# Kernel optimization log

Measured on AMD Instinct MI355X. Metric: run time of the kernel, lower is better.

Reference implementation:

```python
import jax, jax.numpy as jnp
import numpy as np
import math

N_HEADS = 16


def setup_inputs() -> dict:
    key = jax.random.key(0)
    ks = jax.random.split(key, 6)
    B, S, D = 2, 2048, 2048
    hd = D // N_HEADS  # 128
    scale = 0.02
    x = jax.random.normal(ks[0], (B, S, D), dtype=jnp.float32)
    wq = jax.random.normal(ks[1], (D, D), dtype=jnp.float32) * scale
    wk = jax.random.normal(ks[2], (D, D), dtype=jnp.float32) * scale
    wv = jax.random.normal(ks[3], (D, D), dtype=jnp.float32) * scale
    wo = jax.random.normal(ks[4], (D, D), dtype=jnp.float32) * scale
    # Rotary frequencies: theta = 10000^(-2i/hd), angle[t, i] = t * theta_i
    inv_freq = 1.0 / (10000.0 ** (jnp.arange(0, hd, 2, dtype=jnp.float32) / hd))  # [hd//2]
    angles = jnp.arange(S, dtype=jnp.float32)[:, None] * inv_freq[None, :]  # [S, hd//2]
    freqs_cos = jnp.cos(angles)
    freqs_sin = jnp.sin(angles)
    # Causal additive mask [1,1,S,S]
    causal = jnp.tril(jnp.ones((S, S), dtype=bool))
    mask = jnp.where(causal, 0.0, -1e9).astype(jnp.float32)[None, None]
    return {"x": x, "wq": wq, "wk": wk, "wv": wv, "wo": wo,
            "freqs_cos": freqs_cos, "freqs_sin": freqs_sin, "mask": mask}


def _apply_rope(t, cos, sin):
    # t: [B,S,H,hd]; cos/sin: [S, hd//2]. Complex mult on (even, odd) pairs.
    B, S, H, hd = t.shape
    tr = t.reshape(B, S, H, hd // 2, 2)
    t0, t1 = tr[..., 0], tr[..., 1]
    c = cos[None, :, None, :]
    s = sin[None, :, None, :]
    o0 = t0 * c - t1 * s
    o1 = t0 * s + t1 * c
    return jnp.stack([o0, o1], axis=-1).reshape(B, S, H, hd)


def reference(x, wq, wk, wv, wo, freqs_cos, freqs_sin, mask):
    B, S, D = x.shape
    H = N_HEADS
    hd = D // H
    # Projections (torch Linear: y = x @ W^T)
    q = jnp.einsum('bsd,ed->bse', x, wq).reshape(B, S, H, hd)
    k = jnp.einsum('bsd,ed->bse', x, wk).reshape(B, S, H, hd)
    v = jnp.einsum('bsd,ed->bse', x, wv).reshape(B, S, H, hd)
    q = _apply_rope(q, freqs_cos, freqs_sin)
    k = _apply_rope(k, freqs_cos, freqs_sin)
    # Attention: scores [B,H,S,S]
    scores = jnp.einsum('bshd,bthd->bhst', q, k) / math.sqrt(hd)
    scores = scores + mask[:, :, :S, :S]
    attn = jax.nn.softmax(scores.astype(jnp.float32), axis=-1).astype(q.dtype)
    out = jnp.einsum('bhst,bthd->bshd', attn, v).reshape(B, S, D)
    return jnp.einsum('bsd,ed->bse', out, wo)
```

## Files before the change

kernel.cpp:

```cpp
#include <hip/hip_runtime.h>

typedef unsigned short u16;
typedef __attribute__((ext_vector_type(8))) short short8;
typedef __attribute__((ext_vector_type(4))) short short4s;
typedef __attribute__((ext_vector_type(4))) float f32x4;

__device__ __forceinline__ u16 f2b(float f) {
  union { float f; unsigned u; } c; c.f = f;
  unsigned u = c.u;
  unsigned r = (u + 0x7FFFu + ((u >> 16) & 1u)) >> 16;
  return (u16)r;
}
__device__ __forceinline__ float b2f(u16 h) {
  union { unsigned u; float f; } c; c.u = ((unsigned)h) << 16;
  return c.f;
}

__device__ __forceinline__ void gload16(const u16* g, u16* l) {
  __builtin_amdgcn_global_load_lds((const __attribute__((address_space(1))) void*)g,
                                   (__attribute__((address_space(3))) void*)l, 16, 0, 0);
}

__device__ __forceinline__ short4s tr16(const u16* p) {
  short4s d;
  asm volatile("ds_read_b64_tr_b16 %0, %1"
               : "=v"(d)
               : "v"((const __attribute__((address_space(3))) u16*)p));
  return d;
}

#define MFMA(a, b, c) __builtin_amdgcn_mfma_f32_16x16x32_bf16(a, b, c, 0, 0, 0)

__global__ __launch_bounds__(256) void cast_all(const float* __restrict__ x,
                                                const float* __restrict__ wq,
                                                const float* __restrict__ wk,
                                                const float* __restrict__ wv,
                                                const float* __restrict__ wo,
                                                u16* __restrict__ xb,
                                                u16* __restrict__ wqkv,
                                                u16* __restrict__ wob) {
  int i = blockIdx.x * 256 + threadIdx.x;
  const float4* s; u16* d; int off;
  if (i < 2097152)      { s = (const float4*)x;  d = xb;            off = i; }
  else if (i < 3145728) { s = (const float4*)wq; d = wqkv;          off = i - 2097152; }
  else if (i < 4194304) { s = (const float4*)wk; d = wqkv + 4194304; off = i - 3145728; }
  else if (i < 5242880) { s = (const float4*)wv; d = wqkv + 8388608; off = i - 4194304; }
  else                  { s = (const float4*)wo; d = wob;           off = i - 5242880; }
  float4 v = s[off];
  ushort4 r;
  r.x = f2b(v.x); r.y = f2b(v.y); r.z = f2b(v.z); r.w = f2b(v.w);
  *(ushort4*)(d + (size_t)off * 4) = r;
}

__global__ __launch_bounds__(256) void rope_k(u16* __restrict__ qkv,
                                              const float* __restrict__ fc,
                                              const float* __restrict__ fs) {
  int idx = blockIdx.x * 256 + threadIdx.x;
  int m = idx >> 8;
  int c = idx & 255;
  int s = m & 2047;
  int i0 = (c * 4) & 63;
  u16* p = qkv + (size_t)m * 6144 + 2048 + c * 8;
  short8 v = *(short8*)p;
  float4 cs = *(const float4*)(fc + (size_t)s * 64 + i0);
  float4 sn = *(const float4*)(fs + (size_t)s * 64 + i0);
  float cc[4] = {cs.x, cs.y, cs.z, cs.w};
  float ss[4] = {sn.x, sn.y, sn.z, sn.w};
#pragma unroll
  for (int t = 0; t < 4; ++t) {
    float x0 = b2f((u16)v[2 * t]);
    float x1 = b2f((u16)v[2 * t + 1]);
    float o0 = x0 * cc[t] - x1 * ss[t];
    float o1 = x0 * ss[t] + x1 * cc[t];
    v[2 * t]     = (short)f2b(o0);
    v[2 * t + 1] = (short)f2b(o1);
  }
  *(short8*)p = v;
}

template <int F32OUT>
__global__ __launch_bounds__(512, 2) void gemm_wide(const u16* __restrict__ Ag,
                                                    const u16* __restrict__ Bg,
                                                    void* __restrict__ Cp,
                                                    int M, int N, int K) {
  __shared__ __align__(16) u16 lds[40960];
  const int tid = threadIdx.x;
  const int l = tid & 63, w = tid >> 6;
  const int wm = w >> 2, wn = w & 3;
  const int ln = l & 15, lk = l >> 4;
  const int nbn = N / 384;
  const int nwg = (M >> 8) * nbn;
  const int wg = ((blockIdx.x & 7) * (nwg >> 3)) + (blockIdx.x >> 3);
  const int row0 = (wg / nbn) << 8;
  const int col0 = (wg % nbn) * 384;
  const int T = K >> 5;

#define STAGE_A(t)                                                                     \
  {                                                                                    \
    _Pragma("unroll")                                                                  \
    for (int u = 0; u < 2; ++u) {                                                      \
      int e = u * 512 + tid;                                                           \
      int rr = e >> 2;                                                                 \
      gload16(Ag + (size_t)(row0 + rr) * K + (t) * 32 +                                \
                  (((e & 3) ^ ((rr >> 1) & 3)) << 3),                                  \
              lds + ((t) & 1) * 8192 + e * 8);                                         \
    }                                                                                  \
  }
#define STAGE_B(t)                                                                     \
  {                                                                                    \
    _Pragma("unroll")                                                                  \
    for (int u = 0; u < 3; ++u) {                                                      \
      int e = u * 512 + tid;                                                           \
      int rr = e >> 2;                                                                 \
      gload16(Bg + (size_t)(col0 + rr) * K + (t) * 32 +                                \
                  (((e & 3) ^ ((rr >> 1) & 3)) << 3),                                  \
              lds + 16384 + ((t) & 1) * 12288 + e * 8);                                \
    }                                                                                  \
  }

  f32x4 acc[8][6];
#pragma unroll
  for (int m = 0; m < 8; ++m)
#pragma unroll
    for (int n = 0; n < 6; ++n) acc[m][n] = (f32x4){0.f, 0.f, 0.f, 0.f};

  const int cx = (lk ^ ((ln >> 1) & 3)) << 3;

  STAGE_B(0); STAGE_A(0); STAGE_B(1);
  asm volatile("s_waitcnt vmcnt(3)" ::: "memory");
  __builtin_amdgcn_s_barrier();

  for (int t = 0; t < T; ++t) {
    const u16* aB = lds + (t & 1) * 8192;
    const u16* bB = lds + 16384 + (t & 1) * 12288;
    short8 bf[6];
    short8 af[4];

#pragma unroll
    for (int n = 0; n < 6; ++n)
      bf[n] = *(const short8*)&bB[(wn * 96 + n * 16 + ln) * 32 + cx];
#pragma unroll
    for (int mf = 0; mf < 4; ++mf)
      af[mf] = *(const short8*)&aB[(wm * 128 + mf * 16 + ln) * 32 + cx];
    if (t + 1 < T) STAGE_A(t + 1);
    __builtin_amdgcn_s_setprio(1);
#pragma unroll
    for (int mf = 0; mf < 4; ++mf)
#pragma unroll
      for (int n = 0; n < 6; ++n)
        acc[mf][n] = MFMA(af[mf], bf[n], acc[mf][n]);
    __builtin_amdgcn_s_setprio(0);
    __builtin_amdgcn_s_barrier();

#pragma unroll
    for (int mf = 0; mf < 4; ++mf)
      af[mf] = *(const short8*)&aB[(wm * 128 + (4 + mf) * 16 + ln) * 32 + cx];
    if (t + 2 < T) STAGE_B(t + 2);
    __builtin_amdgcn_s_setprio(1);
#pragma unroll
    for (int mf = 0; mf < 4; ++mf)
#pragma unroll
      for (int n = 0; n < 6; ++n)
        acc[4 + mf][n] = MFMA(af[mf], bf[n], acc[4 + mf][n]);
    __builtin_amdgcn_s_setprio(0);
    if (t + 2 < T) { asm volatile("s_waitcnt vmcnt(3)" ::: "memory"); }
    else           { asm volatile("s_waitcnt vmcnt(0)" ::: "memory"); }
    __builtin_amdgcn_s_barrier();
  }

#pragma unroll
  for (int m = 0; m < 8; ++m) {
    int r0 = row0 + wm * 128 + m * 16 + lk * 4;
#pragma unroll
    for (int n = 0; n < 6; ++n) {
      int cc = col0 + wn * 96 + n * 16 + ln;
#pragma unroll
      for (int j = 0; j < 4; ++j) {
        float v = acc[m][n][j];
        if (F32OUT) ((float*)Cp)[(size_t)(r0 + j) * N + cc] = v;
        else        ((u16*)Cp)[(size_t)(r0 + j) * N + cc]   = f2b(v);
      }
    }
  }
#undef STAGE_A
#undef STAGE_B
}

template <int NREP, int F32OUT>
__global__ __launch_bounds__(512, 2) void gemm_big(const u16* __restrict__ Ag,
                                                   const u16* __restrict__ Bg,
                                                   void* __restrict__ Cp,
                                                   int M, int N, int K) {
  __shared__ __align__(16) u16 lds[32768 + NREP * 8192];
  const int tid = threadIdx.x;
  const int l = tid & 63, w = tid >> 6;
  const int wm = w >> 2, wn = w & 3;
  const int ln = l & 15, lk = l >> 4;
  const int BN = NREP * 64;
  const int nbn = N / BN;
  const int nwg = (M >> 8) * nbn;
  const int wg = ((blockIdx.x & 7) * (nwg >> 3)) + (blockIdx.x >> 3);
  const int row0 = (wg / nbn) << 8;
  const int col0 = (wg % nbn) * BN;
  const int T = K >> 6;

#define STAGE_A(t, h)                                                                  \
  {                                                                                    \
    _Pragma("unroll")                                                                  \
    for (int u = 0; u < 2; ++u) {                                                      \
      int e = u * 512 + tid;                                                           \
      int rr = (h) * 128 + (e >> 3);                                                   \
      gload16(Ag + (size_t)(row0 + rr) * K + (t) * 64 + (((e & 7) ^ (rr & 7)) << 3),   \
              lds + ((t) & 1) * 16384 + (h) * 8192 + e * 8);                           \
    }                                                                                  \
  }
#define STAGE_B(t, pb)                                                                 \
  {                                                                                    \
    int rr = (pb) * 64 + (tid >> 3);                                                   \
    gload16(Bg + (size_t)(col0 + rr) * K + (t) * 64 + (((tid & 7) ^ (rr & 7)) << 3),   \
            lds + 32768 + ((t) & 1) * NREP * 4096 + (pb) * 4096 + tid * 8);            \
  }

  f32x4 acc[8][NREP];
#pragma unroll
  for (int m = 0; m < 8; ++m)
#pragma unroll
    for (int n = 0; n < NREP; ++n) acc[m][n] = (f32x4){0.f, 0.f, 0.f, 0.f};

  const int x = ln & 7;
  const int c0 = (lk ^ x) << 3;
  const int c1 = ((4 + lk) ^ x) << 3;

#pragma unroll
  for (int pb = 0; pb < NREP; ++pb) STAGE_B(0, pb);
  STAGE_A(0, 0); STAGE_A(0, 1);
#pragma unroll
  for (int pb = 0; pb < NREP; ++pb) STAGE_B(1, pb);
  asm volatile("s_waitcnt vmcnt(2)" ::: "memory");
  __builtin_amdgcn_s_barrier();

  for (int t = 0; t < T; ++t) {
    const u16* aB = lds + (t & 1) * 16384 + wm * 8192;
    const u16* bB = lds + 32768 + (t & 1) * NREP * 4096;
    short8 bf[NREP][2];
#pragma unroll
    for (int p = 0; p < 4; ++p) {
      if (p == 0) {
#pragma unroll
        for (int n = 0; n < NREP; ++n) {
          int rb = (wn * NREP * 16 + n * 16 + ln) * 64;
          bf[n][0] = *(const short8*)&bB[rb + c0];
          bf[n][1] = *(const short8*)&bB[rb + c1];
        }
      }
      short8 af[2][2];
#pragma unroll
      for (int m2 = 0; m2 < 2; ++m2) {
        int ra = ((p * 2 + m2) * 16 + ln) * 64;
        af[m2][0] = *(const short8*)&aB[ra + c0];
        af[m2][1] = *(const short8*)&aB[ra + c1];
      }
      if (p == 0)      { if (t + 1 < T) STAGE_A(t + 1, 0); }
      else if (p == 1) { if (t + 1 < T) STAGE_A(t + 1, 1);
                         if (t + 2 < T) STAGE_B(t + 2, 0); }
      else if (p == 2) { if (t + 2 < T) STAGE_B(t + 2, 1); }

      __builtin_amdgcn_s_setprio(1);
#pragma unroll
      for (int m2 = 0; m2 < 2; ++m2)
#pragma unroll
        for (int n = 0; n < NREP; ++n)
#pragma unroll
          for (int kk = 0; kk < 2; ++kk)
            acc[p * 2 + m2][n] = MFMA(af[m2][kk], bf[n][kk], acc[p * 2 + m2][n]);
      __builtin_amdgcn_s_setprio(0);

      if (p == 3) {
        if (t + 2 < T)      { asm volatile("s_waitcnt vmcnt(2)" ::: "memory"); }
        else if (t + 1 < T) { asm volatile("s_waitcnt vmcnt(0)" ::: "memory"); }
      }
      __builtin_amdgcn_s_barrier();
    }
  }

#pragma unroll
  for (int m = 0; m < 8; ++m) {
    int r0 = row0 + wm * 128 + m * 16 + lk * 4;
#pragma unroll
    for (int n = 0; n < NREP; ++n) {
      int cc = col0 + wn * NREP * 16 + n * 16 + ln;
#pragma unroll
      for (int j = 0; j < 4; ++j) {
        float v = acc[m][n][j];
        if (F32OUT) ((float*)Cp)[(size_t)(r0 + j) * N + cc] = v;
        else        ((u16*)Cp)[(size_t)(r0 + j) * N + cc]   = f2b(v);
      }
    }
  }
#undef STAGE_A
#undef STAGE_B
}

__global__ __launch_bounds__(512) void attn_fwd(const u16* __restrict__ qkv,
                                                const float* __restrict__ fc,
                                                const float* __restrict__ fs,
                                                u16* __restrict__ out) {
  __shared__ __align__(16) u16 sK[2][64 * 128];
  __shared__ __align__(16) u16 sV[2][64 * 128];
  __shared__ __align__(16) u16 sP[8][16 * 72];
  const int tid = threadIdx.x, l = tid & 63, w = tid >> 6;
  const int ln = l & 15, lk = l >> 4;

  const int bid = blockIdx.x;
  const int l0 = ((bid & 7) << 5) | (bid >> 3);
  const int bh = l0 >> 3, pr = l0 & 7;
  const int b = bh >> 4, h = bh & 15;

  const u16* Kp = qkv + (size_t)b * 2048 * 6144 + 2048 + h * 128;
  const u16* Vp = Kp + 2048;
  const float scale = 0.08838834764831845f;

  for (int pass = 0; pass < 2; ++pass) {
    const int qt = pass ? (15 - pr) : pr;
    const int m0 = b * 2048 + qt * 128;
    const u16* Qp = qkv + (size_t)m0 * 6144 + h * 128;
    const int srow = qt * 128 + w * 16 + ln;

    short8 qf[4];
#pragma unroll
    for (int kc = 0; kc < 4; ++kc) {
      short8 raw = *(const short8*)(Qp + (size_t)(w * 16 + ln) * 6144 + kc * 32 + lk * 8);
      float4 c4 = *(const float4*)(fc + (size_t)srow * 64 + kc * 16 + lk * 4);
      float4 s4 = *(const float4*)(fs + (size_t)srow * 64 + kc * 16 + lk * 4);
      float cc[4] = {c4.x * scale, c4.y * scale, c4.z * scale, c4.w * scale};
      float ss[4] = {s4.x * scale, s4.y * scale, s4.z * scale, s4.w * scale};
#pragma unroll
      for (int t = 0; t < 4; ++t) {
        float x0 = b2f((u16)raw[2 * t]);
        float x1 = b2f((u16)raw[2 * t + 1]);
        qf[kc][2 * t]     = (short)f2b(x0 * cc[t] - x1 * ss[t]);
        qf[kc][2 * t + 1] = (short)f2b(x0 * ss[t] + x1 * cc[t]);
      }
    }

    f32x4 o[8];
#pragma unroll
    for (int d = 0; d < 8; ++d) o[d] = (f32x4){0.f, 0.f, 0.f, 0.f};
    float mrow[4] = {-1e9f, -1e9f, -1e9f, -1e9f};
    float lsum[4] = {0.f, 0.f, 0.f, 0.f};

    const int ntl = 2 * qt + 2;

    {
#pragma unroll
      for (int q = 0; q < 2; ++q) {
        int e = q * 512 + tid;
        int r = e >> 4, p = e & 15;
        gload16(Kp + (size_t)r * 6144 + ((p ^ (r & 7)) << 3), &sK[0][e * 8]);
        int j = ((e >> 6) << 2) + ((e & 7) >> 1);
        int d = (((e >> 3) & 7) << 4) + ((e & 1) << 3);
        gload16(Vp + (size_t)j * 6144 + d, &sV[0][e * 8]);
      }
    }
    __syncthreads();

    int cur = 0;
    for (int jt = 0; jt < ntl; ++jt) {
      if (jt + 1 < ntl) {
        const u16* Kt = Kp + (size_t)(jt + 1) * 64 * 6144;
        const u16* Vt = Vp + (size_t)(jt + 1) * 64 * 6144;
        int nb = cur ^ 1;
#pragma unroll
        for (int q = 0; q < 2; ++q) {
          int e = q * 512 + tid;
          int r = e >> 4, p = e & 15;
          gload16(Kt + (size_t)r * 6144 + ((p ^ (r & 7)) << 3), &sK[nb][e * 8]);
          int j = ((e >> 6) << 2) + ((e & 7) >> 1);
          int d = (((e >> 3) & 7) << 4) + ((e & 1) << 3);
          gload16(Vt + (size_t)j * 6144 + d, &sV[nb][e * 8]);
        }
      }

      f32x4 sf[4];
      __builtin_amdgcn_s_setprio(1);
#pragma unroll
      for (int nc = 0; nc < 4; ++nc) {
        f32x4 s = (f32x4){0.f, 0.f, 0.f, 0.f};
#pragma unroll
        for (int kc = 0; kc < 4; ++kc) {
          int r = nc * 16 + ln;
          short8 kb = *(const short8*)&sK[cur][r * 128 + (((kc << 2) + lk) ^ (r & 7)) * 8];
          s = MFMA(qf[kc], kb, s);
        }
        sf[nc] = s;
      }
      __builtin_amdgcn_s_setprio(0);

      if (jt >= 2 * qt) {
        int ig = qt * 128 + w * 16 + lk * 4;
#pragma unroll
        for (int nc = 0; nc < 4; ++nc) {
          int jg = jt * 64 + nc * 16 + ln;
#pragma unroll
          for (int j = 0; j < 4; ++j)
            sf[nc][j] = (jg > ig + j) ? -1e9f : sf[nc][j];
        }
      }

      float tm[4];
#pragma unroll
      for (int j = 0; j < 4; ++j)
        tm[j] = fmaxf(fmaxf(sf[0][j], sf[1][j]), fmaxf(sf[2][j], sf[3][j]));
      int ok = (tm[0] <= mrow[0] + 8.f) & (tm[1] <= mrow[1] + 8.f) &
               (tm[2] <= mrow[2] + 8.f) & (tm[3] <= mrow[3] + 8.f);
      if (!__all(ok)) {
#pragma unroll
        for (int off = 1; off < 16; off <<= 1)
#pragma unroll
          for (int j = 0; j < 4; ++j) tm[j] = fmaxf(tm[j], __shfl_xor(tm[j], off, 16));
        float al[4];
#pragma unroll
        for (int j = 0; j < 4; ++j) {
          float nm = fmaxf(mrow[j], tm[j]);
          al[j] = __expf(mrow[j] - nm);
          mrow[j] = nm;
        }
#pragma unroll
        for (int d = 0; d < 8; ++d)
#pragma unroll
          for (int j = 0; j < 4; ++j) o[d][j] *= al[j];
#pragma unroll
        for (int j = 0; j < 4; ++j) lsum[j] *= al[j];
      }

#pragma unroll
      for (int nc = 0; nc < 4; ++nc)
#pragma unroll
        for (int j = 0; j < 4; ++j) {
          float p = __expf(sf[nc][j] - mrow[j]);
          u16 pb = f2b(p);
          sP[w][(lk * 4 + j) * 72 + nc * 16 + ln] = pb;
          lsum[j] += b2f(pb);
        }

      short8 pa0 = *(const short8*)&sP[w][ln * 72 + lk * 8];
      short8 pa1 = *(const short8*)&sP[w][ln * 72 + 32 + lk * 8];
      asm volatile("s_waitcnt lgkmcnt(0)" ::: "memory");
      __builtin_amdgcn_sched_barrier(0);

      short4s tb[4][4];
#define TRISSUE(dblk, slot)                                                  \
      {                                                                      \
        const u16* vb = &sV[cur][(lk * 2) * 512 + (dblk) * 64 + ln * 4];     \
        tb[slot][0] = tr16(vb);                                              \
        tb[slot][1] = tr16(vb + 512);                                        \
        tb[slot][2] = tr16(vb + 4096);                                       \
        tb[slot][3] = tr16(vb + 4096 + 512);                                 \
      }
      TRISSUE(0, 0);
      TRISSUE(1, 1);
      __builtin_amdgcn_s_setprio(1);
#pragma unroll
      for (int d = 0; d < 8; ++d) {
        if (d < 6) TRISSUE(d + 2, (d + 2) & 3);
        if (d < 6)       asm volatile("s_waitcnt lgkmcnt(8)" ::: "memory");
        else if (d == 6) asm volatile("s_waitcnt lgkmcnt(4)" ::: "memory");
        else             asm volatile("s_waitcnt lgkmcnt(0)" ::: "memory");
        __builtin_amdgcn_sched_barrier(0);
        short8 vb0 = {tb[d & 3][0][0], tb[d & 3][0][1], tb[d & 3][0][2], tb[d & 3][0][3],
                      tb[d & 3][1][0], tb[d & 3][1][1], tb[d & 3][1][2], tb[d & 3][1][3]};
        short8 vb1 = {tb[d & 3][2][0], tb[d & 3][2][1], tb[d & 3][2][2], tb[d & 3][2][3],
                      tb[d & 3][3][0], tb[d & 3][3][1], tb[d & 3][3][2], tb[d & 3][3][3]};
        o[d] = MFMA(pa0, vb0, o[d]);
        o[d] = MFMA(pa1, vb1, o[d]);
      }
      __builtin_amdgcn_s_setprio(0);
#undef TRISSUE

      __syncthreads();
      cur ^= 1;
    }

#pragma unroll
    for (int off = 1; off < 16; off <<= 1)
#pragma unroll
      for (int j = 0; j < 4; ++j) lsum[j] += __shfl_xor(lsum[j], off, 16);
    float inv[4];
#pragma unroll
    for (int j = 0; j < 4; ++j) inv[j] = 1.f / lsum[j];
#pragma unroll
    for (int d = 0; d < 8; ++d)
#pragma unroll
      for (int j = 0; j < 4; ++j)
        out[(size_t)(m0 + w * 16 + lk * 4 + j) * 2048 + h * 128 + d * 16 + ln] =
            f2b(o[d][j] * inv[j]);
  }
}

extern "C" void kernel_launch(void* const* d_in, const int* in_sizes, int n_in,
                              void* d_out, int out_size, void* d_ws, size_t ws_size,
                              hipStream_t stream) {
  const float* x  = (const float*)d_in[0];
  const float* wq = (const float*)d_in[1];
  const float* wk = (const float*)d_in[2];
  const float* wv = (const float*)d_in[3];
  const float* wo = (const float*)d_in[4];
  const float* fc = (const float*)d_in[5];
  const float* fs = (const float*)d_in[6];

  char* ws = (char*)d_ws;
  u16* xb   = (u16*)(ws);
  u16* wqkv = (u16*)(ws + 16777216);
  u16* wob  = (u16*)(ws + 41943040);
  u16* qkv  = (u16*)(ws + 50331648);
  u16* aout = (u16*)(ws + 100663296);

  cast_all<<<24576, 256, 0, stream>>>(x, wq, wk, wv, wo, xb, wqkv, wob);
  gemm_wide<0><<<256, 512, 0, stream>>>(xb, wqkv, qkv, 4096, 6144, 2048);
  rope_k<<<4096, 256, 0, stream>>>(qkv, fc, fs);
  attn_fwd<<<256, 512, 0, stream>>>(qkv, fc, fs, aout);
  gemm_big<2, 1><<<256, 512, 0, stream>>>(aout, wob, d_out, 4096, 2048, 2048);
}
```

Baseline: 239.8 us.

## Split attention into one block per query tile with single-buffered K

The attention kernel now launches one block per (batch, head, query tile) instead of pairing two tiles per block, ordering heavy tiles first. K is single-buffered with a mid-loop barrier before its next-tile prefetch, which cuts LDS use so more blocks fit per CU (launch_bounds min-blocks hint of 4). The P tile is written with the library bf16 conversion and lsum accumulates unrounded p. This trades more blocks and an extra barrier per iteration for higher occupancy and better load balance, and normalisation differs slightly from the rounded P used in the MFMA.

```diff
diff --git a/kernel.cpp b/kernel.cpp
--- a/kernel.cpp
+++ b/kernel.cpp
@@ -1,4 +1,5 @@
 #include <hip/hip_runtime.h>
+#include <hip/hip_bf16.h>
 
 typedef unsigned short u16;
 typedef __attribute__((ext_vector_type(8))) short short8;
@@ -301,200 +302,209 @@
 #undef STAGE_B
 }
 
-__global__ __launch_bounds__(512) void attn_fwd(const u16* __restrict__ qkv,
-                                                const float* __restrict__ fc,
-                                                const float* __restrict__ fs,
-                                                u16* __restrict__ out) {
-  __shared__ __align__(16) u16 sK[2][64 * 128];
+__global__ __launch_bounds__(512, 4) void attn_fwd(const u16* __restrict__ qkv,
+                                                   const float* __restrict__ fc,
+                                                   const float* __restrict__ fs,
+                                                   u16* __restrict__ out) {
+  __shared__ __align__(16) u16 sK[64 * 128];
   __shared__ __align__(16) u16 sV[2][64 * 128];
   __shared__ __align__(16) u16 sP[8][16 * 72];
   const int tid = threadIdx.x, l = tid & 63, w = tid >> 6;
   const int ln = l & 15, lk = l >> 4;
 
   const int bid = blockIdx.x;
-  const int l0 = ((bid & 7) << 5) | (bid >> 3);
-  const int bh = l0 >> 3, pr = l0 & 7;
+  const int l0 = ((bid & 7) << 6) | (bid >> 3);
+  const int bh = l0 >> 4;
+  const int qt = 15 - (l0 & 15);
   const int b = bh >> 4, h = bh & 15;
 
   const u16* Kp = qkv + (size_t)b * 2048 * 6144 + 2048 + h * 128;
   const u16* Vp = Kp + 2048;
   const float scale = 0.08838834764831845f;
 
-  for (int pass = 0; pass < 2; ++pass) {
-    const int qt = pass ? (15 - pr) : pr;
-    const int m0 = b * 2048 + qt * 128;
-    const u16* Qp = qkv + (size_t)m0 * 6144 + h * 128;
-    const int srow = qt * 128 + w * 16 + ln;
-
-    short8 qf[4];
-#pragma unroll
-    for (int kc = 0; kc < 4; ++kc) {
-      short8 raw = *(const short8*)(Qp + (size_t)(w * 16 + ln) * 6144 + kc * 32 + lk * 8);
-      float4 c4 = *(const float4*)(fc + (size_t)srow * 64 + kc * 16 + lk * 4);
-      float4 s4 = *(const float4*)(fs + (size_t)srow * 64 + kc * 16 + lk * 4);
-      float cc[4] = {c4.x * scale, c4.y * scale, c4.z * scale, c4.w * scale};
-      float ss[4] = {s4.x * scale, s4.y * scale, s4.z * scale, s4.w * scale};
-#pragma unroll
-      for (int t = 0; t < 4; ++t) {
-        float x0 = b2f((u16)raw[2 * t]);
-        float x1 = b2f((u16)raw[2 * t + 1]);
-        qf[kc][2 * t]     = (short)f2b(x0 * cc[t] - x1 * ss[t]);
-        qf[kc][2 * t + 1] = (short)f2b(x0 * ss[t] + x1 * cc[t]);
-      }
-    }
-
-    f32x4 o[8];
-#pragma unroll
-    for (int d = 0; d < 8; ++d) o[d] = (f32x4){0.f, 0.f, 0.f, 0.f};
-    float mrow[4] = {-1e9f, -1e9f, -1e9f, -1e9f};
-    float lsum[4] = {0.f, 0.f, 0.f, 0.f};
-
-    const int ntl = 2 * qt + 2;
-
-    {
+  const int m0 = b * 2048 + qt * 128;
+  const u16* Qp = qkv + (size_t)m0 * 6144 + h * 128;
+  const int srow = qt * 128 + w * 16 + ln;
+
+  short8 qf[4];
+#pragma unroll
+  for (int kc = 0; kc < 4; ++kc) {
+    short8 raw = *(const short8*)(Qp + (size_t)(w * 16 + ln) * 6144 + kc * 32 + lk * 8);
+    float4 c4 = *(const float4*)(fc + (size_t)srow * 64 + kc * 16 + lk * 4);
+    float4 s4 = *(const float4*)(fs + (size_t)srow * 64 + kc * 16 + lk * 4);
+    float cc[4] = {c4.x * scale, c4.y * scale, c4.z * scale, c4.w * scale};
+    float ss[4] = {s4.x * scale, s4.y * scale, s4.z * scale, s4.w * scale};
+#pragma unroll
+    for (int t = 0; t < 4; ++t) {
+      float x0 = b2f((u16)raw[2 * t]);
+      float x1 = b2f((u16)raw[2 * t + 1]);
+      qf[kc][2 * t]     = (short)f2b(x0 * cc[t] - x1 * ss[t]);
+      qf[kc][2 * t + 1] = (short)f2b(x0 * ss[t] + x1 * cc[t]);
+    }
+  }
+
+  f32x4 o[8];
+#pragma unroll
+  for (int d = 0; d < 8; ++d) o[d] = (f32x4){0.f, 0.f, 0.f, 0.f};
+  float mrow[4] = {-1e9f, -1e9f, -1e9f, -1e9f};
+  float lsum[4] = {0.f, 0.f, 0.f, 0.f};
+
+  const int ntl = 2 * qt + 2;
+
+  {
+#pragma unroll
+    for (int q = 0; q < 2; ++q) {
+      int e = q * 512 + tid;
+      int r = e >> 4, p = e & 15;
+      gload16(Kp + (size_t)r * 6144 + ((p ^ (r & 7)) << 3), &sK[e * 8]);
+      int j = ((e >> 6) << 2) + ((e & 7) >> 1);
+      int d = (((e >> 3) & 7) << 4) + ((e & 1) << 3);
+      gload16(Vp + (size_t)j * 6144 + d, &sV[0][e * 8]);
+    }
+  }
+  __syncthreads();
+
+  int cur = 0;
+  for (int jt = 0; jt < ntl; ++jt) {
+    if (jt + 1 < ntl) {
+      const u16* Vt = Vp + (size_t)(jt + 1) * 64 * 6144;
+      int nb = cur ^ 1;
+#pragma unroll
+      for (int q = 0; q < 2; ++q) {
+        int e = q * 512 + tid;
+        int j = ((e >> 6) << 2) + ((e & 7) >> 1);
+        int d = (((e >> 3) & 7) << 4) + ((e & 1) << 3);
+        gload16(Vt + (size_t)j * 6144 + d, &sV[nb][e * 8]);
+      }
+    }
+
+    f32x4 sf[4];
+    __builtin_amdgcn_s_setprio(1);
+#pragma unroll
+    for (int nc = 0; nc < 4; ++nc) {
+      f32x4 s = (f32x4){0.f, 0.f, 0.f, 0.f};
+#pragma unroll
+      for (int kc = 0; kc < 4; ++kc) {
+        int r = nc * 16 + ln;
+        short8 kb = *(const short8*)&sK[r * 128 + (((kc << 2) + lk) ^ (r & 7)) * 8];
+        s = MFMA(qf[kc], kb, s);
+      }
+      sf[nc] = s;
+    }
+    __builtin_amdgcn_s_setprio(0);
+
+    __builtin_amdgcn_sched_barrier(0);
+    __builtin_amdgcn_s_barrier();
+    __builtin_amdgcn_sched_barrier(0);
+    if (jt + 1 < ntl) {
+      const u16* Kt = Kp + (size_t)(jt + 1) * 64 * 6144;
 #pragma unroll
       for (int q = 0; q < 2; ++q) {
         int e = q * 512 + tid;
         int r = e >> 4, p = e & 15;
-        gload16(Kp + (size_t)r * 6144 + ((p ^ (r & 7)) << 3), &sK[0][e * 8]);
-        int j = ((e >> 6) << 2) + ((e & 7) >> 1);
-        int d = (((e >> 3) & 7) << 4) + ((e & 1) << 3);
-        gload16(Vp + (size_t)j * 6144 + d, &sV[0][e * 8]);
-      }
-    }
+        gload16(Kt + (size_t)r * 6144 + ((p ^ (r & 7)) << 3), &sK[e * 8]);
+      }
+    }
+
+    if (jt >= 2 * qt) {
+      int ig = qt * 128 + w * 16 + lk * 4;
+#pragma unroll
+      for (int nc = 0; nc < 4; ++nc) {
+        int jg = jt * 64 + nc * 16 + ln;
+#pragma unroll
+        for (int j = 0; j < 4; ++j)
+          sf[nc][j] = (jg > ig + j) ? -1e9f : sf[nc][j];
+      }
+    }
+
+    float tm[4];
+#pragma unroll
+    for (int j = 0; j < 4; ++j)
+      tm[j] = fmaxf(fmaxf(sf[0][j], sf[1][j]), fmaxf(sf[2][j], sf[3][j]));
+    int ok = (tm[0] <= mrow[0] + 8.f) & (tm[1] <= mrow[1] + 8.f) &
+             (tm[2] <= mrow[2] + 8.f) & (tm[3] <= mrow[3] + 8.f);
+    if (!__all(ok)) {
+#pragma unroll
+      for (int off = 1; off < 16; off <<= 1)
+#pragma unroll
+        for (int j = 0; j < 4; ++j) tm[j] = fmaxf(tm[j], __shfl_xor(tm[j], off, 16));
+      float al[4];
+#pragma unroll
+      for (int j = 0; j < 4; ++j) {
+        float nm = fmaxf(mrow[j], tm[j]);
+        al[j] = __expf(mrow[j] - nm);
+        mrow[j] = nm;
+      }
+#pragma unroll
+      for (int d = 0; d < 8; ++d)
+#pragma unroll
+        for (int j = 0; j < 4; ++j) o[d][j] *= al[j];
+#pragma unroll
+      for (int j = 0; j < 4; ++j) lsum[j] *= al[j];
+    }
+
+    short4s tb[4][4];
+#define TRISSUE(dblk, slot)                                                  \
+    {                                                                        \
+      const u16* vb = &sV[cur][(lk * 2) * 512 + (dblk) * 64 + ln * 4];       \
+      tb[slot][0] = tr16(vb);                                                \
+      tb[slot][1] = tr16(vb + 512);                                          \
+      tb[slot][2] = tr16(vb + 4096);                                         \
+      tb[slot][3] = tr16(vb + 4096 + 512);                                   \
+    }
+    TRISSUE(0, 0);
+    TRISSUE(1, 1);
+
+#pragma unroll
+    for (int nc = 0; nc < 4; ++nc)
+#pragma unroll
+      for (int j = 0; j < 4; ++j) {
+        float p = __expf(sf[nc][j] - mrow[j]);
+        __hip_bfloat16 hb = __float2bfloat16(p);
+        sP[w][(lk * 4 + j) * 72 + nc * 16 + ln] = *(u16*)&hb;
+        lsum[j] += p;
+      }
+
+    short8 pa0 = *(const short8*)&sP[w][ln * 72 + lk * 8];
+    short8 pa1 = *(const short8*)&sP[w][ln * 72 + 32 + lk * 8];
+    asm volatile("s_waitcnt lgkmcnt(0)" ::: "memory");
+    __builtin_amdgcn_sched_barrier(0);
+
+    __builtin_amdgcn_s_setprio(1);
+#pragma unroll
+    for (int d = 0; d < 8; ++d) {
+      if (d < 6) TRISSUE(d + 2, (d + 2) & 3);
+      if (d < 6)       asm volatile("s_waitcnt lgkmcnt(8)" ::: "memory");
+      else if (d == 6) asm volatile("s_waitcnt lgkmcnt(4)" ::: "memory");
+      else             asm volatile("s_waitcnt lgkmcnt(0)" ::: "memory");
+      __builtin_amdgcn_sched_barrier(0);
+      short8 vb0 = {tb[d & 3][0][0], tb[d & 3][0][1], tb[d & 3][0][2], tb[d & 3][0][3],
+                    tb[d & 3][1][0], tb[d & 3][1][1], tb[d & 3][1][2], tb[d & 3][1][3]};
+      short8 vb1 = {tb[d & 3][2][0], tb[d & 3][2][1], tb[d & 3][2][2], tb[d & 3][2][3],
+                    tb[d & 3][3][0], tb[d & 3][3][1], tb[d & 3][3][2], tb[d & 3][3][3]};
+      o[d] = MFMA(pa0, vb0, o[d]);
+      o[d] = MFMA(pa1, vb1, o[d]);
+    }
+    __builtin_amdgcn_s_setprio(0);
+#undef TRISSUE
+
     __syncthreads();
-
-    int cur = 0;
-    for (int jt = 0; jt < ntl; ++jt) {
-      if (jt + 1 < ntl) {
-        const u16* Kt = Kp + (size_t)(jt + 1) * 64 * 6144;
-        const u16* Vt = Vp + (size_t)(jt + 1) * 64 * 6144;
-        int nb = cur ^ 1;
-#pragma unroll
-        for (int q = 0; q < 2; ++q) {
-          int e = q * 512 + tid;
-          int r = e >> 4, p = e & 15;
-          gload16(Kt + (size_t)r * 6144 + ((p ^ (r & 7)) << 3), &sK[nb][e * 8]);
-          int j = ((e >> 6) << 2) + ((e & 7) >> 1);
-          int d = (((e >> 3) & 7) << 4) + ((e & 1) << 3);
-          gload16(Vt + (size_t)j * 6144 + d, &sV[nb][e * 8]);
-        }
-      }
-
-      f32x4 sf[4];
-      __builtin_amdgcn_s_setprio(1);
-#pragma unroll
-      for (int nc = 0; nc < 4; ++nc) {
-        f32x4 s = (f32x4){0.f, 0.f, 0.f, 0.f};
-#pragma unroll
-        for (int kc = 0; kc < 4; ++kc) {
-          int r = nc * 16 + ln;
-          short8 kb = *(const short8*)&sK[cur][r * 128 + (((kc << 2) + lk) ^ (r & 7)) * 8];
-          s = MFMA(qf[kc], kb, s);
-        }
-        sf[nc] = s;
-      }
-      __builtin_amdgcn_s_setprio(0);
-
-      if (jt >= 2 * qt) {
-        int ig = qt * 128 + w * 16 + lk * 4;
-#pragma unroll
-        for (int nc = 0; nc < 4; ++nc) {
-          int jg = jt * 64 + nc * 16 + ln;
-#pragma unroll
-          for (int j = 0; j < 4; ++j)
-            sf[nc][j] = (jg > ig + j) ? -1e9f : sf[nc][j];
-        }
-      }
-
-      float tm[4];
-#pragma unroll
-      for (int j = 0; j < 4; ++j)
-        tm[j] = fmaxf(fmaxf(sf[0][j], sf[1][j]), fmaxf(sf[2][j], sf[3][j]));
-      int ok = (tm[0] <= mrow[0] + 8.f) & (tm[1] <= mrow[1] + 8.f) &
-               (tm[2] <= mrow[2] + 8.f) & (tm[3] <= mrow[3] + 8.f);
-      if (!__all(ok)) {
-#pragma unroll
-        for (int off = 1; off < 16; off <<= 1)
-#pragma unroll
-          for (int j = 0; j < 4; ++j) tm[j] = fmaxf(tm[j], __shfl_xor(tm[j], off, 16));
-        float al[4];
-#pragma unroll
-        for (int j = 0; j < 4; ++j) {
-          float nm = fmaxf(mrow[j], tm[j]);
-          al[j] = __expf(mrow[j] - nm);
-          mrow[j] = nm;
-        }
-#pragma unroll
-        for (int d = 0; d < 8; ++d)
-#pragma unroll
-          for (int j = 0; j < 4; ++j) o[d][j] *= al[j];
-#pragma unroll
-        for (int j = 0; j < 4; ++j) lsum[j] *= al[j];
-      }
-
-#pragma unroll
-      for (int nc = 0; nc < 4; ++nc)
-#pragma unroll
-        for (int j = 0; j < 4; ++j) {
-          float p = __expf(sf[nc][j] - mrow[j]);
-          u16 pb = f2b(p);
-          sP[w][(lk * 4 + j) * 72 + nc * 16 + ln] = pb;
-          lsum[j] += b2f(pb);
-        }
-
-      short8 pa0 = *(const short8*)&sP[w][ln * 72 + lk * 8];
-      short8 pa1 = *(const short8*)&sP[w][ln * 72 + 32 + lk * 8];
-      asm volatile("s_waitcnt lgkmcnt(0)" ::: "memory");
-      __builtin_amdgcn_sched_barrier(0);
-
-      short4s tb[4][4];
-#define TRISSUE(dblk, slot)                                                  \
-      {                                                                      \
-        const u16* vb = &sV[cur][(lk * 2) * 512 + (dblk) * 64 + ln * 4];     \
-        tb[slot][0] = tr16(vb);                                              \
-        tb[slot][1] = tr16(vb + 512);                                        \
-        tb[slot][2] = tr16(vb + 4096);                                       \
-        tb[slot][3] = tr16(vb + 4096 + 512);                                 \
-      }
-      TRISSUE(0, 0);
-      TRISSUE(1, 1);
-      __builtin_amdgcn_s_setprio(1);
-#pragma unroll
-      for (int d = 0; d < 8; ++d) {
-        if (d < 6) TRISSUE(d + 2, (d + 2) & 3);
-        if (d < 6)       asm volatile("s_waitcnt lgkmcnt(8)" ::: "memory");
-        else if (d == 6) asm volatile("s_waitcnt lgkmcnt(4)" ::: "memory");
-        else             asm volatile("s_waitcnt lgkmcnt(0)" ::: "memory");
-        __builtin_amdgcn_sched_barrier(0);
-        short8 vb0 = {tb[d & 3][0][0], tb[d & 3][0][1], tb[d & 3][0][2], tb[d & 3][0][3],
-                      tb[d & 3][1][0], tb[d & 3][1][1], tb[d & 3][1][2], tb[d & 3][1][3]};
-        short8 vb1 = {tb[d & 3][2][0], tb[d & 3][2][1], tb[d & 3][2][2], tb[d & 3][2][3],
-                      tb[d & 3][3][0], tb[d & 3][3][1], tb[d & 3][3][2], tb[d & 3][3][3]};
-        o[d] = MFMA(pa0, vb0, o[d]);
-        o[d] = MFMA(pa1, vb1, o[d]);
-      }
-      __builtin_amdgcn_s_setprio(0);
-#undef TRISSUE
-
-      __syncthreads();
-      cur ^= 1;
-    }
-
-#pragma unroll
-    for (int off = 1; off < 16; off <<= 1)
-#pragma unroll
-      for (int j = 0; j < 4; ++j) lsum[j] += __shfl_xor(lsum[j], off, 16);
-    float inv[4];
-#pragma unroll
-    for (int j = 0; j < 4; ++j) inv[j] = 1.f / lsum[j];
-#pragma unroll
-    for (int d = 0; d < 8; ++d)
-#pragma unroll
-      for (int j = 0; j < 4; ++j)
-        out[(size_t)(m0 + w * 16 + lk * 4 + j) * 2048 + h * 128 + d * 16 + ln] =
-            f2b(o[d][j] * inv[j]);
-  }
+    cur ^= 1;
+  }
+
+#pragma unroll
+  for (int off = 1; off < 16; off <<= 1)
+#pragma unroll
+    for (int j = 0; j < 4; ++j) lsum[j] += __shfl_xor(lsum[j], off, 16);
+  float inv[4];
+#pragma unroll
+  for (int j = 0; j < 4; ++j) inv[j] = 1.f / lsum[j];
+#pragma unroll
+  for (int d = 0; d < 8; ++d)
+#pragma unroll
+    for (int j = 0; j < 4; ++j)
+      out[(size_t)(m0 + w * 16 + lk * 4 + j) * 2048 + h * 128 + d * 16 + ln] =
+          f2b(o[d][j] * inv[j]);
 }
 
 extern "C" void kernel_launch(void* const* d_in, const int* in_sizes, int n_in,
@@ -518,6 +528,6 @@
   cast_all<<<24576, 256, 0, stream>>>(x, wq, wk, wv, wo, xb, wqkv, wob);
   gemm_wide<0><<<256, 512, 0, stream>>>(xb, wqkv, qkv, 4096, 6144, 2048);
   rope_k<<<4096, 256, 0, stream>>>(qkv, fc, fs);
-  attn_fwd<<<256, 512, 0, stream>>>(qkv, fc, fs, aout);
+  attn_fwd<<<512, 512, 0, stream>>>(qkv, fc, fs, aout);
   gemm_big<2, 1><<<256, 512, 0, stream>>>(aout, wob, d_out, 4096, 2048, 2048);
 }
```

New measurement: 254.2 us. 1.06x slower.
